# Optimization experiments

Hardware: AMD Instinct MI355X
Metric: run time of the kernel (lower is better)

The kernel has to match this reference:

```python
import jax, jax.numpy as jnp
import numpy as np

EPS = 1e-5  # BatchNorm eps (torch default)

def conv2d(x, w, padding=0, dilation=1):
    # x: NCHW, w: OIHW
    return jax.lax.conv_general_dilated(
        x, w, window_strides=(1, 1),
        padding=[(padding, padding), (padding, padding)],
        rhs_dilation=(dilation, dilation),
        dimension_numbers=('NCHW', 'OIHW', 'NCHW'))

def bn_relu(x, scale, bias):
    # eval-mode BatchNorm with running_mean=0, running_var=1, then ReLU
    inv = scale / np.sqrt(1.0 + EPS)
    return jax.nn.relu(x * inv[None, :, None, None] + bias[None, :, None, None])

def setup_inputs() -> dict:
    key = jax.random.key(0)
    ks = jax.random.split(key, 12)
    B, C, H, W = 4, 512, 64, 64
    def nrm(k, shape, fan):
        return jax.random.normal(k, shape, jnp.float32) * np.sqrt(2.0 / fan)
    return {
        'x': jax.random.normal(ks[0], (B, C, H, W), jnp.float32),
        'w_a1': nrm(ks[1], (128, 512, 1, 1), 1 * 1 * 128),
        'w_a2': nrm(ks[2], (128, 512, 3, 3), 3 * 3 * 128),
        'w_a3': nrm(ks[3], (128, 512, 3, 3), 3 * 3 * 128),
        'w_a4': nrm(ks[4], (128, 512, 3, 3), 3 * 3 * 128),
        'w_a5': nrm(ks[5], (128, 512, 1, 1), 1 * 1 * 128),
        'bn_scale': jnp.ones((5, 128), jnp.float32),
        'bn_bias': jnp.zeros((5, 128), jnp.float32),
        'w_q': jax.random.normal(ks[6], (128, 640, 1, 1), jnp.float32) * 0.04,
        'b_q': jnp.zeros((128,), jnp.float32),
        'w_k': jax.random.normal(ks[7], (128, 640, 1, 1), jnp.float32) * 0.04,
        'b_k': jnp.zeros((128,), jnp.float32),
        'w_v': jax.random.normal(ks[8], (512, 512, 1, 1), jnp.float32) * 0.04,
        'b_v': jnp.zeros((512,), jnp.float32),
        'gamma': jax.random.uniform(ks[9], (1,), jnp.float32),
    }

def reference(x, w_a1, w_a2, w_a3, w_a4, w_a5, bn_scale, bn_bias,
              w_q, b_q, w_k, b_k, w_v, b_v, gamma):
    B, C, H, W = x.shape
    N = H * W
    # ASPP branches (query and key paths use identical weights & input,
    # so compute once and reuse — same math as the original)
    b1 = bn_relu(conv2d(x, w_a1, 0, 1), bn_scale[0], bn_bias[0])
    b2 = bn_relu(conv2d(x, w_a2, 2, 2), bn_scale[1], bn_bias[1])
    b3 = bn_relu(conv2d(x, w_a3, 3, 3), bn_scale[2], bn_bias[2])
    b4 = bn_relu(conv2d(x, w_a4, 6, 6), bn_scale[3], bn_bias[3])
    # aspp5: global avg pool -> 1x1 conv -> BN -> ReLU -> bilinear up to HxW
    # (bilinear upsample of a 1x1 map with align_corners=True is a broadcast)
    p5 = jnp.mean(x, axis=(2, 3), keepdims=True)            # [B,512,1,1]
    p5 = bn_relu(conv2d(p5, w_a5, 0, 1), bn_scale[4], bn_bias[4])
    b5 = jnp.broadcast_to(p5, (B, 128, H, W))
    feat = jnp.concatenate([b1, b2, b3, b4, b5], axis=1)    # [B,640,H,W]

    q = (conv2d(feat, w_q) + b_q[None, :, None, None]).reshape(B, 128, N)  # [B,128,N]
    k = (conv2d(feat, w_k) + b_k[None, :, None, None]).reshape(B, 128, N)  # [B,128,N]
    v = (conv2d(x, w_v) + b_v[None, :, None, None]).reshape(B, C, N)       # [B,C,N]

    energy = jnp.einsum('bcn,bcm->bnm', q, k)               # [B,N,N], unscaled
    attention = jax.nn.softmax(energy, axis=-1)
    out = jnp.einsum('bcm,bnm->bcn', v, attention).reshape(B, C, H, W)
    return gamma[0] * out + x
```

## Files before the change

kernel.cpp:

```cpp
#include <hip/hip_runtime.h>

typedef _Float16 f16x8 __attribute__((ext_vector_type(8)));
typedef _Float16 f16x4 __attribute__((ext_vector_type(4)));
typedef float f32x4 __attribute__((ext_vector_type(4)));

#define N_PIX 4096
#define C_IN  512
#define BN_INV 0.99999500003749969f
#define CCH 64

#define GLOAD_LDS16(g, l)                                        \
  __builtin_amdgcn_global_load_lds(                              \
      (const __attribute__((address_space(1))) void*)(g),        \
      (__attribute__((address_space(3))) void*)(l), 16, 0, 0)

__device__ __forceinline__ f32x4 mfma16(f16x8 a, f16x8 b, f32x4 c) {
  return __builtin_amdgcn_mfma_f32_16x16x32_f16(a, b, c, 0, 0, 0);
}
__device__ __forceinline__ f16x8 ldnt(const _Float16* base, int row, int ld, int k0, int lane) {
  return *(const f16x8*)(base + (size_t)(row + (lane & 15)) * ld + k0 + ((lane >> 4) << 3));
}

__global__ __launch_bounds__(256) void k_xT(const float* __restrict__ x, _Float16* __restrict__ xT) {
  __shared__ float t[32][33];
  int b = blockIdx.z, p0 = blockIdx.x * 32, c0 = blockIdx.y * 32;
  int tx = threadIdx.x & 31, ty = threadIdx.x >> 5;
  const float* xb = x + ((size_t)b * C_IN + c0) * N_PIX + p0;
  for (int i = 0; i < 32; i += 8) t[ty + i][tx] = xb[(size_t)(ty + i) * N_PIX + tx];
  __syncthreads();
  _Float16* o = xT + ((size_t)b * N_PIX + p0) * C_IN + c0;
  for (int i = 0; i < 32; i += 8) o[(size_t)(ty + i) * C_IN + tx] = (_Float16)t[tx][ty + i];
}

__global__ __launch_bounds__(256) void k_f2h4(const float* __restrict__ a, _Float16* __restrict__ oa, int na,
                                              const float* __restrict__ b_, _Float16* __restrict__ ob, int nb,
                                              const float* __restrict__ c, _Float16* __restrict__ oc, int nc,
                                              const float* __restrict__ d, _Float16* __restrict__ od, int nd) {
  int i = blockIdx.x * 256 + threadIdx.x;
  if (i < na) { oa[i] = (_Float16)a[i]; return; }
  i -= na;
  if (i < nb) { ob[i] = (_Float16)b_[i]; return; }
  i -= nb;
  if (i < nc) { oc[i] = (_Float16)c[i]; return; }
  i -= nc;
  if (i < nd) od[i] = (_Float16)d[i];
}

__global__ __launch_bounds__(256) void k_packw(const float* __restrict__ w2, const float* __restrict__ w3,
                                               const float* __restrict__ w4, _Float16* __restrict__ wp) {
  int idx = blockIdx.x * 256 + threadIdx.x;
  int conv = idx / 589824;
  int t1 = idx % 589824;
  int tap = t1 / 65536;
  int t2 = t1 % 65536;
  int oc = t2 / 512, c = t2 % 512;
  const float* w = (conv == 0) ? w2 : (conv == 1) ? w3 : w4;
  wp[idx] = (_Float16)w[(size_t)(oc * 512 + c) * 9 + tap];
}

__global__ __launch_bounds__(256) void k_mean(const float* __restrict__ x, float* __restrict__ meanv) {
  int c = blockIdx.x, b = blockIdx.y;
  const float* p = x + ((size_t)b * C_IN + c) * N_PIX;
  float s = 0.f;
  for (int i = threadIdx.x; i < N_PIX; i += 256) s += p[i];
  for (int off = 32; off; off >>= 1) s += __shfl_down(s, off);
  __shared__ float ls[4];
  if ((threadIdx.x & 63) == 0) ls[threadIdx.x >> 6] = s;
  __syncthreads();
  if (threadIdx.x == 0) meanv[(size_t)b * C_IN + c] = (ls[0] + ls[1] + ls[2] + ls[3]) * (1.f / N_PIX);
}

__global__ void k_p5(const float* __restrict__ w5, const float* __restrict__ meanv,
                     const float* __restrict__ bnS, const float* __restrict__ bnB, _Float16* __restrict__ p5h) {
  int b = blockIdx.x, oc = threadIdx.x;
  const float* m = meanv + (size_t)b * C_IN;
  const float* w = w5 + (size_t)oc * C_IN;
  float s = 0.f;
  for (int c = 0; c < C_IN; ++c) s += w[c] * m[c];
  float v = fmaxf(s * bnS[oc] * BN_INV + bnB[oc], 0.f);
  p5h[b * 128 + oc] = (_Float16)v;
}

__global__ __launch_bounds__(256) void k_b5(const _Float16* __restrict__ p5h, _Float16* __restrict__ featT) {
  int i = blockIdx.x * 256 + threadIdx.x;
  int oc = i & 127, p = (i >> 7) & 4095, b = i >> 19;
  featT[((size_t)b * N_PIX + p) * 640 + 512 + oc] = p5h[b * 128 + oc];
}

__global__ __launch_bounds__(256, 4) void k_conv(const _Float16* __restrict__ xT, const _Float16* __restrict__ w1h,
                                                 const _Float16* __restrict__ wph, const float* __restrict__ bnS,
                                                 const float* __restrict__ bnB, _Float16* __restrict__ featT) {
  __shared__ _Float16 Ap[3 * 76 * CCH];
  int y = blockIdx.x;
  int tb = blockIdx.y;
  int task = tb >> 2, b = tb & 3;
  int tid = threadIdx.x, wid = tid >> 6, lane = tid & 63;
  int dil = (task == 0) ? 0 : (task == 1) ? 2 : (task == 2) ? 3 : 6;
  int ntap = task ? 9 : 1;
  int nrow = task ? 3 : 1;
  const _Float16* wt0 = task ? wph + (size_t)(task - 1) * 9 * 128 * C_IN : w1h;
  f32x4 acc[4][2] = {};

  for (int cc = 0; cc < C_IN / CCH; ++cc) {
    int c0 = cc * CCH;
    __syncthreads();
    if (dil) {
      int nz = nrow * 2 * dil * (CCH / 8);
      for (int i = tid; i < nz; i += 256) {
        int cv = (i & (CCH / 8 - 1)) * 8;
        int t2 = i / (CCH / 8);
        int colh = t2 % (2 * dil);
        int r = t2 / (2 * dil);
        int col = (colh < dil) ? colh : 64 + colh;
        int ba = (((r * 76 + col) * CCH + cv) * 2) ^ ((col & 7) << 4);
        *(f16x8*)((char*)Ap + ba) = (f16x8){};
      }
    }
    int nf = nrow * 64 * (CCH / 8);
    for (int i = tid; i < nf; i += 256) {
      int cv = (i & (CCH / 8 - 1)) * 8;
      int t2 = i / (CCH / 8);
      int px = t2 & 63;
      int r = t2 >> 6;
      int ry = y + (r - 1) * dil;
      f16x8 v = {};
      if ((unsigned)ry < 64u)
        v = *(const f16x8*)(xT + ((size_t)b * N_PIX + ry * 64 + px) * C_IN + c0 + cv);
      int col = dil + px;
      int ba = (((r * 76 + col) * CCH + cv) * 2) ^ ((col & 7) << 4);
      *(f16x8*)((char*)Ap + ba) = v;
    }
    __syncthreads();
    for (int tap = 0; tap < ntap; ++tap) {
      int rsel = tap / 3;
      int dx = (tap % 3 - 1) * dil;
      const _Float16* wt = wt0 + (size_t)tap * 128 * C_IN;
#pragma unroll
      for (int k = 0; k < CCH / 32; ++k) {
        f16x8 wf0 = ldnt(wt, wid * 32, C_IN, c0 + k * 32, lane);
        f16x8 wf1 = ldnt(wt, wid * 32 + 16, C_IN, c0 + k * 32, lane);
        f16x8 af[4];
#pragma unroll
        for (int m = 0; m < 4; ++m) {
          int col = dil + dx + m * 16 + (lane & 15);
          int ch = k * 32 + ((lane >> 4) << 3);
          int ba = (((rsel * 76 + col) * CCH + ch) * 2) ^ ((col & 7) << 4);
          af[m] = *(const f16x8*)((char*)Ap + ba);
        }
#pragma unroll
        for (int m = 0; m < 4; ++m) {
          acc[m][0] = mfma16(af[m], wf0, acc[m][0]);
          acc[m][1] = mfma16(af[m], wf1, acc[m][1]);
        }
      }
    }
  }
  int brOff = task * 128;
  _Float16* F = featT + (size_t)b * N_PIX * 640;
#pragma unroll
  for (int n = 0; n < 2; ++n) {
    int oc = wid * 32 + n * 16 + (lane & 15);
    float inv = bnS[brOff + oc] * BN_INV, bs = bnB[brOff + oc];
#pragma unroll
    for (int m = 0; m < 4; ++m) {
#pragma unroll
      for (int r = 0; r < 4; ++r) {
        int pix = y * 64 + m * 16 + ((lane >> 4) << 2) + r;
        F[(size_t)pix * 640 + brOff + oc] = (_Float16)fmaxf(acc[m][n][r] * inv + bs, 0.f);
      }
    }
  }
}

__global__ __launch_bounds__(256) void k_qk(const _Float16* __restrict__ featT, const _Float16* __restrict__ wqh,
                                            const _Float16* __restrict__ wkh, const float* __restrict__ bq,
                                            const float* __restrict__ bk, _Float16* __restrict__ qT,
                                            _Float16* __restrict__ kT) {
  int b = blockIdx.z, which = blockIdx.y, p0 = blockIdx.x * 32;
  const _Float16* wh = which ? wkh : wqh;
  const float* bias = which ? bk : bq;
  _Float16* oT = which ? kT : qT;
  int tid = threadIdx.x, wid = tid >> 6, lane = tid & 63;
  int pw = wid & 1, ocq = wid >> 1;
  const _Float16* A = featT + (size_t)b * N_PIX * 640;
  int pr = p0 + pw * 16;
  f32x4 acc[4] = {};
  for (int kk = 0; kk < 20; ++kk) {
    f16x8 af = ldnt(A, pr, 640, kk * 32, lane);
#pragma unroll
    for (int nn = 0; nn < 4; ++nn) {
      f16x8 bf = ldnt(wh, ocq * 64 + nn * 16, 640, kk * 32, lane);
      acc[nn] = mfma16(af, bf, acc[nn]);
    }
  }
  _Float16* O = oT + (size_t)b * N_PIX * 128;
#pragma unroll
  for (int nn = 0; nn < 4; ++nn) {
    int oc = ocq * 64 + nn * 16 + (lane & 15);
    float bb = bias[oc];
#pragma unroll
    for (int r = 0; r < 4; ++r) {
      int pix = pr + ((lane >> 4) << 2) + r;
      O[(size_t)pix * 128 + oc] = (_Float16)(acc[nn][r] + bb);
    }
  }
}

__global__ __launch_bounds__(256) void k_v(const _Float16* __restrict__ xT, const _Float16* __restrict__ wvh,
                                           const float* __restrict__ bv, _Float16* __restrict__ vv) {
  int b = blockIdx.z, oc0 = blockIdx.x * 64, p0 = blockIdx.y * 128;
  int tid = threadIdx.x, wid = tid >> 6, lane = tid & 63;
  const _Float16* Bm = xT + (size_t)b * N_PIX * C_IN;
  int or0 = oc0 + wid * 16;
  f32x4 acc[8] = {};
  for (int kk = 0; kk < 16; ++kk) {
    f16x8 af = ldnt(wvh, or0, C_IN, kk * 32, lane);
#pragma unroll
    for (int nn = 0; nn < 8; ++nn) {
      f16x8 bf = ldnt(Bm, p0 + nn * 16, C_IN, kk * 32, lane);
      acc[nn] = mfma16(af, bf, acc[nn]);
    }
  }
  _Float16* V = vv + (size_t)b * C_IN * N_PIX;
#pragma unroll
  for (int r = 0; r < 4; ++r) {
    int oc = or0 + ((lane >> 4) << 2) + r;
    float bb = bv[oc];
#pragma unroll
    for (int nn = 0; nn < 8; ++nn) {
      int pix = p0 + nn * 16 + (lane & 15);
      V[(size_t)oc * N_PIX + pix] = (_Float16)(acc[nn][r] + bb);
    }
  }
}

__global__ __launch_bounds__(512, 2) void k_attn(const _Float16* __restrict__ qT, const _Float16* __restrict__ kT,
                                                 const _Float16* __restrict__ vv, const float* __restrict__ x,
                                                 const float* __restrict__ gamma, float* __restrict__ out) {
  __shared__ _Float16 Kb[2][128 * 128];
  __shared__ _Float16 P[64 * 128];
  __shared__ float fbuf[64];
  int b = blockIdx.y, n0 = blockIdx.x * 64;
  int tid = threadIdx.x, wid = tid >> 6, lane = tid & 63;
  const _Float16* Q = qT + (size_t)b * N_PIX * 128;
  const _Float16* K = kT + (size_t)b * N_PIX * 128;
  const _Float16* V = vv + (size_t)b * C_IN * N_PIX;
  float g = gamma[0];
  f16x8 qf[4];
  int n_local = (wid & 3) * 16 + (lane & 15);
  if (wid < 4) {
#pragma unroll
    for (int kk = 0; kk < 4; ++kk) qf[kk] = ldnt(Q, n0 + wid * 16, 128, kk * 32, lane);
  }
  float m_run = -3.4e38f, sm = 0.f;
  f32x4 acc[4][4] = {};

  auto stageK = [&](int it, int buf) {
    const _Float16* src = K + (size_t)it * 128 * 128;
    int cs = (lane & 15) << 4;
#pragma unroll
    for (int i = 0; i < 4; ++i) {
      int rr = wid * 16 + i * 4 + (lane >> 4);
      const char* gp = (const char*)(src + (size_t)rr * 128) + (cs ^ ((rr & 7) << 4));
      char* lp = (char*)&Kb[buf][0] + (size_t)(wid * 16 + i * 4) * 256;
      GLOAD_LDS16(gp, lp);
    }
  };

  auto phaseA = [&](int kbuf) {
    const char* kb = (const char*)&Kb[kbuf][0];
    f32x4 s8[8];
#pragma unroll
    for (int mm = 0; mm < 8; ++mm) {
      int row = mm * 16 + (lane & 15);
      int kboff = (lane >> 4) << 4;
      f32x4 s = {};
#pragma unroll
      for (int kk = 0; kk < 4; ++kk) {
        f16x8 kf = *(const f16x8*)(kb + (size_t)row * 256 + ((kk * 64 + kboff) ^ ((row & 7) << 4)));
        s = mfma16(kf, qf[kk], s);
      }
      s8[mm] = s;
    }
    float tmx = s8[0][0];
#pragma unroll
    for (int mm = 0; mm < 8; ++mm) {
      tmx = fmaxf(tmx, fmaxf(fmaxf(s8[mm][0], s8[mm][1]), fmaxf(s8[mm][2], s8[mm][3])));
    }
    tmx = fmaxf(tmx, __shfl_xor(tmx, 16));
    tmx = fmaxf(tmx, __shfl_xor(tmx, 32));
    float f = 1.f;
    if (tmx > m_run + 8.f) {
      f = __expf(m_run - tmx);
      m_run = tmx;
    }
    sm *= f;
    if (lane < 16) fbuf[n_local] = f;
#pragma unroll
    for (int mm = 0; mm < 8; ++mm) {
      f16x4 pv;
#pragma unroll
      for (int r = 0; r < 4; ++r) {
        float p = __expf(s8[mm][r] - m_run);
        sm += p;
        pv[r] = (_Float16)p;
      }
      int m_local = mm * 16 + ((lane >> 4) << 2);
      *(f16x4*)((char*)P + (size_t)n_local * 256 + ((m_local * 2) ^ ((n_local & 7) << 4))) = pv;
    }
  };

  auto phaseB = [&](int it) {
    float f[4];
#pragma unroll
    for (int nn = 0; nn < 4; ++nn) f[nn] = fbuf[nn * 16 + (lane & 15)];
    bool need = (f[0] != 1.f) | (f[1] != 1.f) | (f[2] != 1.f) | (f[3] != 1.f);
    if (__any(need)) {
#pragma unroll
      for (int cc = 0; cc < 4; ++cc)
#pragma unroll
        for (int nn = 0; nn < 4; ++nn) acc[cc][nn] = acc[cc][nn] * f[nn];
    }
#pragma unroll
    for (int k2 = 0; k2 < 4; ++k2) {
      f16x8 pb[4];
#pragma unroll
      for (int nn = 0; nn < 4; ++nn) {
        int n = nn * 16 + (lane & 15);
        int mbyte = k2 * 64 + ((lane >> 4) << 4);
        pb[nn] = *(const f16x8*)((char*)P + (size_t)n * 256 + (mbyte ^ ((n & 7) << 4)));
      }
#pragma unroll
      for (int cc = 0; cc < 4; ++cc) {
        f16x8 af = ldnt(V, wid * 64 + cc * 16, N_PIX, it * 128 + k2 * 32, lane);
#pragma unroll
        for (int nn = 0; nn < 4; ++nn) acc[cc][nn] = mfma16(af, pb[nn], acc[cc][nn]);
      }
    }
  };

  stageK(0, 0);
  __syncthreads();
  for (int it = 0; it < 32; ++it) {
    if (it < 31) stageK(it + 1, (it + 1) & 1);
    if (wid < 4) phaseA(it & 1);
    __syncthreads();
    phaseB(it);
    __syncthreads();
  }

  if (wid < 4) {
    float st = sm;
    st += __shfl_xor(st, 16);
    st += __shfl_xor(st, 32);
    if (lane < 16) fbuf[n_local] = st;
  }
  __syncthreads();
  float inv_s[4];
#pragma unroll
  for (int nn = 0; nn < 4; ++nn)
    inv_s[nn] = 1.f / fbuf[nn * 16 + (lane & 15)];
#pragma unroll
  for (int cc = 0; cc < 4; ++cc) {
#pragma unroll
    for (int r = 0; r < 4; ++r) {
      int oc = wid * 64 + cc * 16 + ((lane >> 4) << 2) + r;
#pragma unroll
      for (int nn = 0; nn < 4; ++nn) {
        int pix = n0 + nn * 16 + (lane & 15);
        size_t idx = ((size_t)(b * C_IN + oc)) * N_PIX + pix;
        out[idx] = fmaf(g * inv_s[nn], acc[cc][nn][r], x[idx]);
      }
    }
  }
}

extern "C" void kernel_launch(void* const* d_in, const int* in_sizes, int n_in,
                              void* d_out, int out_size, void* d_ws, size_t ws_size,
                              hipStream_t stream) {
  const float* x = (const float*)d_in[0];
  const float* wa1 = (const float*)d_in[1];
  const float* wa2 = (const float*)d_in[2];
  const float* wa3 = (const float*)d_in[3];
  const float* wa4 = (const float*)d_in[4];
  const float* wa5 = (const float*)d_in[5];
  const float* bnS = (const float*)d_in[6];
  const float* bnB = (const float*)d_in[7];
  const float* wq = (const float*)d_in[8];
  const float* bq = (const float*)d_in[9];
  const float* wk = (const float*)d_in[10];
  const float* bk = (const float*)d_in[11];
  const float* wv = (const float*)d_in[12];
  const float* bv = (const float*)d_in[13];
  const float* gamma = (const float*)d_in[14];

  char* ws = (char*)d_ws;
  size_t off = 0;
  auto alloc = [&](size_t bytes) -> char* {
    char* p = ws + off;
    off = (off + bytes + 255) & ~(size_t)255;
    return p;
  };
  _Float16* xT = (_Float16*)alloc((size_t)4 * 4096 * 512 * 2);
  _Float16* featT = (_Float16*)alloc((size_t)4 * 4096 * 640 * 2);
  _Float16* qT = (_Float16*)alloc((size_t)4 * 4096 * 128 * 2);
  _Float16* kT = (_Float16*)alloc((size_t)4 * 4096 * 128 * 2);
  _Float16* vvp = (_Float16*)alloc((size_t)4 * 512 * 4096 * 2);
  _Float16* w1h = (_Float16*)alloc((size_t)128 * 512 * 2);
  _Float16* wph = (_Float16*)alloc((size_t)3 * 9 * 128 * 512 * 2);
  _Float16* wqh = (_Float16*)alloc((size_t)128 * 640 * 2);
  _Float16* wkh = (_Float16*)alloc((size_t)128 * 640 * 2);
  _Float16* wvh = (_Float16*)alloc((size_t)512 * 512 * 2);
  float* meanv = (float*)alloc((size_t)4 * 512 * 4);
  _Float16* p5h = (_Float16*)alloc((size_t)4 * 128 * 2);
  if (off > ws_size) return;

  float* out = (float*)d_out;

  hipLaunchKernelGGL(k_xT, dim3(128, 16, 4), dim3(256), 0, stream, x, xT);
  hipLaunchKernelGGL(k_f2h4, dim3(1920), dim3(256), 0, stream, wa1, w1h, 65536, wq, wqh, 81920, wk, wkh, 81920,
                     wv, wvh, 262144);
  hipLaunchKernelGGL(k_packw, dim3(6912), dim3(256), 0, stream, wa2, wa3, wa4, wph);
  hipLaunchKernelGGL(k_mean, dim3(512, 4), dim3(256), 0, stream, x, meanv);
  hipLaunchKernelGGL(k_p5, dim3(4), dim3(128), 0, stream, wa5, meanv, bnS + 4 * 128, bnB + 4 * 128, p5h);
  hipLaunchKernelGGL(k_b5, dim3(8192), dim3(256), 0, stream, p5h, featT);
  hipLaunchKernelGGL(k_conv, dim3(64, 16), dim3(256), 0, stream, xT, w1h, wph, bnS, bnB, featT);
  hipLaunchKernelGGL(k_qk, dim3(128, 2, 4), dim3(256), 0, stream, featT, wqh, wkh, bq, bk, qT, kT);
  hipLaunchKernelGGL(k_v, dim3(8, 32, 4), dim3(256), 0, stream, xT, wvh, bv, vvp);
  hipLaunchKernelGGL(k_attn, dim3(64, 4), dim3(512), 0, stream, qT, kT, vvp, x, gamma, out);
}
```

Measured before the change: 455.9 us.

## Warp-specialize attention: softmax waves produce P while MFMA waves consume

Splits the attention block into producer waves (QK^T plus online softmax into a double-buffered P tile) and consumer waves (PV MFMA over 128 channels each), so the softmax of step it+1 overlaps the PV product of step it. It adds a K prefetch two steps ahead, a second P and scale buffer, priority raising around the MFMA loop, and removes one barrier per iteration. Consumer waves now hold twice the accumulators (128 floats per lane), which raises register pressure and may spill under the 512x2 launch bounds. Only half the waves issue PV MFMAs.

```diff
diff --git a/kernel.cpp b/kernel.cpp
--- a/kernel.cpp
+++ b/kernel.cpp
@@ -238,8 +238,9 @@
                                                  const _Float16* __restrict__ vv, const float* __restrict__ x,
                                                  const float* __restrict__ gamma, float* __restrict__ out) {
   __shared__ _Float16 Kb[2][128 * 128];
-  __shared__ _Float16 P[64 * 128];
-  __shared__ float fbuf[64];
+  __shared__ _Float16 P[2][64 * 128];
+  __shared__ float fbuf[2][64];
+  __shared__ float sbuf[64];
   int b = blockIdx.y, n0 = blockIdx.x * 64;
   int tid = threadIdx.x, wid = tid >> 6, lane = tid & 63;
   const _Float16* Q = qT + (size_t)b * N_PIX * 128;
@@ -253,7 +254,11 @@
     for (int kk = 0; kk < 4; ++kk) qf[kk] = ldnt(Q, n0 + wid * 16, 128, kk * 32, lane);
   }
   float m_run = -3.4e38f, sm = 0.f;
-  f32x4 acc[4][4] = {};
+  f32x4 acc[8][4];
+#pragma unroll
+  for (int cc = 0; cc < 8; ++cc)
+#pragma unroll
+    for (int nn = 0; nn < 4; ++nn) acc[cc][nn] = (f32x4){};
 
   auto stageK = [&](int it, int buf) {
     const _Float16* src = K + (size_t)it * 128 * 128;
@@ -267,8 +272,9 @@
     }
   };
 
-  auto phaseA = [&](int kbuf) {
-    const char* kb = (const char*)&Kb[kbuf][0];
+  auto phaseA = [&](int it) {
+    int buf = it & 1;
+    const char* kb = (const char*)&Kb[buf][0];
     f32x4 s8[8];
 #pragma unroll
     for (int mm = 0; mm < 8; ++mm) {
@@ -284,9 +290,8 @@
     }
     float tmx = s8[0][0];
 #pragma unroll
-    for (int mm = 0; mm < 8; ++mm) {
+    for (int mm = 0; mm < 8; ++mm)
       tmx = fmaxf(tmx, fmaxf(fmaxf(s8[mm][0], s8[mm][1]), fmaxf(s8[mm][2], s8[mm][3])));
-    }
     tmx = fmaxf(tmx, __shfl_xor(tmx, 16));
     tmx = fmaxf(tmx, __shfl_xor(tmx, 32));
     float f = 1.f;
@@ -295,7 +300,7 @@
       m_run = tmx;
     }
     sm *= f;
-    if (lane < 16) fbuf[n_local] = f;
+    if (lane < 16) fbuf[buf][n_local] = f;
 #pragma unroll
     for (int mm = 0; mm < 8; ++mm) {
       f16x4 pv;
@@ -306,18 +311,20 @@
         pv[r] = (_Float16)p;
       }
       int m_local = mm * 16 + ((lane >> 4) << 2);
-      *(f16x4*)((char*)P + (size_t)n_local * 256 + ((m_local * 2) ^ ((n_local & 7) << 4))) = pv;
+      *(f16x4*)((char*)&P[buf][0] + (size_t)n_local * 256 + ((m_local * 2) ^ ((n_local & 7) << 4))) = pv;
     }
   };
 
   auto phaseB = [&](int it) {
+    int buf = it & 1;
+    int c0 = (wid - 4) * 128;
     float f[4];
 #pragma unroll
-    for (int nn = 0; nn < 4; ++nn) f[nn] = fbuf[nn * 16 + (lane & 15)];
+    for (int nn = 0; nn < 4; ++nn) f[nn] = fbuf[buf][nn * 16 + (lane & 15)];
     bool need = (f[0] != 1.f) | (f[1] != 1.f) | (f[2] != 1.f) | (f[3] != 1.f);
     if (__any(need)) {
 #pragma unroll
-      for (int cc = 0; cc < 4; ++cc)
+      for (int cc = 0; cc < 8; ++cc)
 #pragma unroll
         for (int nn = 0; nn < 4; ++nn) acc[cc][nn] = acc[cc][nn] * f[nn];
     }
@@ -328,24 +335,31 @@
       for (int nn = 0; nn < 4; ++nn) {
         int n = nn * 16 + (lane & 15);
         int mbyte = k2 * 64 + ((lane >> 4) << 4);
-        pb[nn] = *(const f16x8*)((char*)P + (size_t)n * 256 + (mbyte ^ ((n & 7) << 4)));
-      }
-#pragma unroll
-      for (int cc = 0; cc < 4; ++cc) {
-        f16x8 af = ldnt(V, wid * 64 + cc * 16, N_PIX, it * 128 + k2 * 32, lane);
+        pb[nn] = *(const f16x8*)((char*)&P[buf][0] + (size_t)n * 256 + (mbyte ^ ((n & 7) << 4)));
+      }
+      __builtin_amdgcn_s_setprio(1);
+#pragma unroll
+      for (int cc = 0; cc < 8; ++cc) {
+        f16x8 af = ldnt(V, c0 + cc * 16, N_PIX, it * 128 + k2 * 32, lane);
 #pragma unroll
         for (int nn = 0; nn < 4; ++nn) acc[cc][nn] = mfma16(af, pb[nn], acc[cc][nn]);
       }
+      __builtin_amdgcn_s_setprio(0);
     }
   };
 
   stageK(0, 0);
+  stageK(1, 1);
+  __syncthreads();
+  if (wid < 4) phaseA(0);
   __syncthreads();
   for (int it = 0; it < 32; ++it) {
-    if (it < 31) stageK(it + 1, (it + 1) & 1);
-    if (wid < 4) phaseA(it & 1);
-    __syncthreads();
-    phaseB(it);
+    if (it < 30) stageK(it + 2, it & 1);
+    if (wid < 4) {
+      if (it < 31) phaseA(it + 1);
+    } else {
+      phaseB(it);
+    }
     __syncthreads();
   }
 
@@ -353,23 +367,25 @@
     float st = sm;
     st += __shfl_xor(st, 16);
     st += __shfl_xor(st, 32);
-    if (lane < 16) fbuf[n_local] = st;
+    if (lane < 16) sbuf[n_local] = st;
   }
   __syncthreads();
-  float inv_s[4];
-#pragma unroll
-  for (int nn = 0; nn < 4; ++nn)
-    inv_s[nn] = 1.f / fbuf[nn * 16 + (lane & 15)];
-#pragma unroll
-  for (int cc = 0; cc < 4; ++cc) {
-#pragma unroll
-    for (int r = 0; r < 4; ++r) {
-      int oc = wid * 64 + cc * 16 + ((lane >> 4) << 2) + r;
-#pragma unroll
-      for (int nn = 0; nn < 4; ++nn) {
-        int pix = n0 + nn * 16 + (lane & 15);
-        size_t idx = ((size_t)(b * C_IN + oc)) * N_PIX + pix;
-        out[idx] = fmaf(g * inv_s[nn], acc[cc][nn][r], x[idx]);
+  if (wid >= 4) {
+    int c0 = (wid - 4) * 128;
+    float inv_s[4];
+#pragma unroll
+    for (int nn = 0; nn < 4; ++nn) inv_s[nn] = 1.f / sbuf[nn * 16 + (lane & 15)];
+#pragma unroll
+    for (int cc = 0; cc < 8; ++cc) {
+#pragma unroll
+      for (int r = 0; r < 4; ++r) {
+        int oc = c0 + cc * 16 + ((lane >> 4) << 2) + r;
+#pragma unroll
+        for (int nn = 0; nn < 4; ++nn) {
+          int pix = n0 + nn * 16 + (lane & 15);
+          size_t idx = ((size_t)(b * C_IN + oc)) * N_PIX + pix;
+          out[idx] = fmaf(g * inv_s[nn], acc[cc][nn][r], x[idx]);
+        }
       }
     }
   }
```

New measurement: 448.4 us. Within noise of the previous version (-1.6%).
